# Kernel optimization log

Measured on AMD Instinct MI355X. Metric: run time of the kernel, lower is better.

The kernel has to match this reference:

```python
import jax, jax.numpy as jnp
import numpy as np

B, S, E = 2, 2048, 1024
H, BLK = 16, 32
HD = E // H


def setup_inputs() -> dict:
    key = jax.random.key(0)
    ks = jax.random.split(key, 9)
    s = 1.0 / np.sqrt(E)
    return {
        "x": jax.random.normal(ks[0], (B, S, E), dtype=jnp.float32),
        "Wq": jax.random.normal(ks[1], (E, E), dtype=jnp.float32) * s,
        "bq": jnp.zeros((E,), dtype=jnp.float32),
        "Wk": jax.random.normal(ks[2], (E, E), dtype=jnp.float32) * s,
        "bk": jnp.zeros((E,), dtype=jnp.float32),
        "Wv": jax.random.normal(ks[3], (E, E), dtype=jnp.float32) * s,
        "bv": jnp.zeros((E,), dtype=jnp.float32),
        "Wo": jax.random.normal(ks[4], (E, E), dtype=jnp.float32) * s,
        "bo": jnp.zeros((E,), dtype=jnp.float32),
    }


def reference(x, Wq, bq, Wk, bk, Wv, bv, Wo, bo):
    b, s, e = x.shape
    # projections (torch Linear: x @ W.T + b), split heads -> [b, h, s, hd]
    def proj(W, bias):
        return (x @ W.T + bias).reshape(b, s, H, HD).transpose(0, 2, 1, 3)

    q = proj(Wq, bq)
    k = proj(Wk, bk)
    v = proj(Wv, bv)

    scale = 1.0 / np.sqrt(HD)
    scores = jnp.einsum("bhqd,bhkd->bhqk", q, k) * scale  # [b,h,s,s]

    # block-causal mask: query block i attends to all key blocks j <= i
    idx = jnp.arange(s)
    allowed = (idx[None, :] // BLK) <= (idx[:, None] // BLK)  # [s, s]
    scores = jnp.where(allowed[None, None], scores, jnp.float32(-1e9))

    probs = jax.nn.softmax(scores, axis=-1)
    attn = jnp.einsum("bhqk,bhkd->bhqd", probs, v)  # [b,h,s,hd]
    out = attn.transpose(0, 2, 1, 3).reshape(b, s, e)
    return out @ Wo.T + bo
```

## Files before the change

kernel.cpp:

```cpp
#include <hip/hip_runtime.h>
#include <hip/hip_bf16.h>
#include <stdint.h>

#define BATCH 2
#define S_LEN 2048
#define EMB   1024
#define NHEAD 16
#define HDIM  64

typedef __attribute__((ext_vector_type(8)))  __bf16 bf16x8;
typedef __attribute__((ext_vector_type(4)))  __bf16 bf16x4;
typedef __attribute__((ext_vector_type(4)))  float  f32x4;
typedef __attribute__((ext_vector_type(16))) float  f32x16;

#define ZERO16 ((f32x16){0.f,0.f,0.f,0.f,0.f,0.f,0.f,0.f,0.f,0.f,0.f,0.f,0.f,0.f,0.f,0.f})
#define SM_SCALE_LOG2 0.18033688011112042f

static __device__ __forceinline__ void gload_lds16(const void* g, void* l) {
    __builtin_amdgcn_global_load_lds(
        (__attribute__((address_space(1))) void*)g,
        (__attribute__((address_space(3))) void*)l,
        16, 0, 0);
}

__global__ void f2b_all(const float* __restrict__ x,
                        const float* __restrict__ Wq, const float* __restrict__ Wk,
                        const float* __restrict__ Wv, const float* __restrict__ Wo,
                        __bf16* __restrict__ xb,
                        __bf16* __restrict__ wqb, __bf16* __restrict__ wkb,
                        __bf16* __restrict__ wvb, __bf16* __restrict__ wob) {
    int i = blockIdx.x * blockDim.x + threadIdx.x;
    const float* s;
    __bf16* d;
    int off;
    if (i < (1 << 20)) {
        s = x; d = xb; off = i;
    } else {
        int r   = i - (1 << 20);
        int seg = r >> 18;
        off = r & ((1 << 18) - 1);
        s = seg == 0 ? Wq : seg == 1 ? Wk : seg == 2 ? Wv : Wo;
        d = seg == 0 ? wqb : seg == 1 ? wkb : seg == 2 ? wvb : wob;
    }
    float4 v = reinterpret_cast<const float4*>(s)[off];
    bf16x4 o = { (__bf16)v.x, (__bf16)v.y, (__bf16)v.z, (__bf16)v.w };
    reinterpret_cast<bf16x4*>(d)[off] = o;
}

__global__ __launch_bounds__(256)
void gemm_o64(const __bf16* __restrict__ A, const __bf16* __restrict__ W,
              const float* __restrict__ bias, float* __restrict__ out,
              int M, int N, int K) {
    __shared__ __align__(16) __bf16 As[2][128 * 64];
    __shared__ __align__(16) __bf16 Bs[2][64 * 64];

    const int t    = threadIdx.x;
    const int w    = t >> 6;
    const int lane = t & 63;
    const int m0   = blockIdx.y * 128;
    const int n0   = blockIdx.x * 64;
    const int wr   = w * 32;
    const int fr   = lane & 15;
    const int g16  = lane >> 4;

    f32x4 acc[2][4];
#pragma unroll
    for (int i = 0; i < 2; ++i)
#pragma unroll
        for (int n = 0; n < 4; ++n) acc[i][n] = (f32x4){0.f, 0.f, 0.f, 0.f};

    auto stage = [&](int kt, int buf) {
#pragma unroll
        for (int i = 0; i < 4; ++i) {
            int chunk = i * 256 + t;
            int row   = chunk >> 3;
            int col   = ((chunk & 7) ^ (row & 7)) * 8;
            gload_lds16(A + (size_t)(m0 + row) * K + kt + col,
                        (char*)&As[buf][0] + i * 4096 + w * 1024);
        }
#pragma unroll
        for (int i = 0; i < 2; ++i) {
            int chunk = i * 256 + t;
            int row   = chunk >> 3;
            int col   = ((chunk & 7) ^ (row & 7)) * 8;
            gload_lds16(W + (size_t)(n0 + row) * K + kt + col,
                        (char*)&Bs[buf][0] + i * 4096 + w * 1024);
        }
    };

    stage(0, 0);
    __syncthreads();

    const int NK = K / 64;
    for (int k6 = 0; k6 < NK; ++k6) {
        const int cur = k6 & 1;
        if (k6 + 1 < NK) stage((k6 + 1) * 64, cur ^ 1);

#pragma unroll
        for (int kh = 0; kh < 2; ++kh) {
            bf16x8 af[2], bfv[4];
#pragma unroll
            for (int m = 0; m < 2; ++m) {
                int row = wr + m * 16 + fr;
                int cg  = ((4 * kh + g16) ^ (row & 7)) * 8;
                af[m] = *(const bf16x8*)&As[cur][row * 64 + cg];
            }
#pragma unroll
            for (int n = 0; n < 4; ++n) {
                int row = n * 16 + fr;
                int cg  = ((4 * kh + g16) ^ (row & 7)) * 8;
                bfv[n] = *(const bf16x8*)&Bs[cur][row * 64 + cg];
            }
#pragma unroll
            for (int m = 0; m < 2; ++m)
#pragma unroll
                for (int n = 0; n < 4; ++n)
                    acc[m][n] = __builtin_amdgcn_mfma_f32_16x16x32_bf16(
                        af[m], bfv[n], acc[m][n], 0, 0, 0);
        }
        __syncthreads();
    }

    const int rbase = (lane >> 4) * 4;
#pragma unroll
    for (int m = 0; m < 2; ++m) {
#pragma unroll
        for (int n = 0; n < 4; ++n) {
            int col  = n0 + n * 16 + fr;
            float bv = bias[col];
#pragma unroll
            for (int jj = 0; jj < 4; ++jj) {
                int row = m0 + wr + m * 16 + rbase + jj;
                out[(size_t)row * N + col] = acc[m][n][jj] + bv;
            }
        }
    }
}

__global__ __launch_bounds__(512)
void gemm_qkv(const __bf16* __restrict__ xb,
              const __bf16* __restrict__ Wqb, const __bf16* __restrict__ Wkb,
              const __bf16* __restrict__ Wvb,
              const float* __restrict__ bqp, const float* __restrict__ bkp,
              const float* __restrict__ bvp,
              __bf16* __restrict__ Qo, __bf16* __restrict__ Ko,
              __bf16* __restrict__ VTo, int K) {
    __shared__ __align__(16) __bf16 As[2][128 * 64];
    __shared__ __align__(16) __bf16 Bs[2][128 * 64];

    const int which = blockIdx.x >> 3;
    const int xx    = blockIdx.x & 7;

    const __bf16* Ap;
    const __bf16* Wp;
    int m0, n0;
    if (which == 2) {
        Ap = Wvb; Wp = xb;
        m0 = xx * 128;
        n0 = blockIdx.y * 128;
    } else {
        Ap = xb; Wp = (which == 0) ? Wqb : Wkb;
        m0 = blockIdx.y * 128;
        n0 = xx * 128;
    }
    const float* bias = which == 0 ? bqp : which == 1 ? bkp : bvp;

    const int t    = threadIdx.x;
    const int w    = t >> 6;
    const int lane = t & 63;
    const int wr   = (w >> 2) * 64;
    const int wc   = (w & 3) * 32;
    const int fr   = lane & 15;
    const int g16  = lane >> 4;

    f32x4 acc[4][2];
#pragma unroll
    for (int i = 0; i < 4; ++i)
#pragma unroll
        for (int j = 0; j < 2; ++j) acc[i][j] = (f32x4){0.f, 0.f, 0.f, 0.f};

    auto stage = [&](int kt, int buf) {
#pragma unroll
        for (int i = 0; i < 2; ++i) {
            int chunk = i * 512 + t;
            int row   = chunk >> 3;
            int col   = ((chunk & 7) ^ (row & 7)) * 8;
            gload_lds16(Ap + (size_t)(m0 + row) * K + kt + col,
                        (char*)&As[buf][0] + i * 8192 + w * 1024);
            gload_lds16(Wp + (size_t)(n0 + row) * K + kt + col,
                        (char*)&Bs[buf][0] + i * 8192 + w * 1024);
        }
    };

    stage(0, 0);
    __syncthreads();

    const int NK = K / 64;
    for (int k6 = 0; k6 < NK; ++k6) {
        const int cur = k6 & 1;
        if (k6 + 1 < NK) stage((k6 + 1) * 64, cur ^ 1);

#pragma unroll
        for (int kh = 0; kh < 2; ++kh) {
            bf16x8 af[4], bfv[2];
#pragma unroll
            for (int m = 0; m < 4; ++m) {
                int row = wr + m * 16 + fr;
                int cg  = ((4 * kh + g16) ^ (row & 7)) * 8;
                af[m] = *(const bf16x8*)&As[cur][row * 64 + cg];
            }
#pragma unroll
            for (int n = 0; n < 2; ++n) {
                int row = wc + n * 16 + fr;
                int cg  = ((4 * kh + g16) ^ (row & 7)) * 8;
                bfv[n] = *(const bf16x8*)&Bs[cur][row * 64 + cg];
            }
#pragma unroll
            for (int m = 0; m < 4; ++m)
#pragma unroll
                for (int n = 0; n < 2; ++n)
                    acc[m][n] = __builtin_amdgcn_mfma_f32_16x16x32_bf16(
                        af[m], bfv[n], acc[m][n], 0, 0, 0);
        }
        __syncthreads();
    }

    const int rbase = (lane >> 4) * 4;
    if (which == 2) {
#pragma unroll
        for (int m = 0; m < 4; ++m) {
#pragma unroll
            for (int n = 0; n < 2; ++n) {
                int col = n0 + wc + n * 16 + fr;
                int b   = col >> 11, s = col & (S_LEN - 1);
#pragma unroll
                for (int jj = 0; jj < 4; ++jj) {
                    int row = m0 + wr + m * 16 + rbase + jj;
                    int hh  = row >> 6, d = row & (HDIM - 1);
                    float v = acc[m][n][jj] + bias[row];
                    VTo[(((size_t)(b * NHEAD + hh)) * HDIM + d) * S_LEN + s] = (__bf16)v;
                }
            }
        }
    } else {
        __bf16* outp = (which == 0) ? Qo : Ko;
#pragma unroll
        for (int m = 0; m < 4; ++m) {
#pragma unroll
            for (int n = 0; n < 2; ++n) {
                int col  = n0 + wc + n * 16 + fr;
                float bv = bias[col];
#pragma unroll
                for (int jj = 0; jj < 4; ++jj) {
                    int row = m0 + wr + m * 16 + rbase + jj;
                    float v = acc[m][n][jj] + bv;
                    int b = row >> 11, s = row & (S_LEN - 1);
                    int hh = col >> 6, d = col & (HDIM - 1);
                    outp[(((size_t)(b * NHEAD + hh)) * S_LEN + s) * HDIM + d] = (__bf16)v;
                }
            }
        }
    }
}

__global__ __launch_bounds__(512, 4)
void attn10_kernel(const __bf16* __restrict__ Q, const __bf16* __restrict__ Kv,
                   const __bf16* __restrict__ VT, __bf16* __restrict__ out) {
    __shared__ __align__(16) char smem[51200];
    __bf16* Kt0 = (__bf16*)smem;
    __bf16* Vt  = (__bf16*)(smem + 32768);
    float*  bc  = (float*)(smem + 49152);

    const int t    = threadIdx.x;
    const int w8   = t >> 6;
    const int lane = t & 63;
    const int h    = lane >> 5;
    const int q32  = lane & 31;
    const int j    = w8 & 3;
    const int h2   = w8 >> 2;
    const int bh   = blockIdx.x;
    const int yy   = blockIdx.y;
    const int qt   = (yy < 8) ? (15 - yy) : (yy - 8);
    const int qb   = 4 * qt + j;
    const int C    = qt + 1;

    const __bf16* Qp  = Q  + (size_t)bh * S_LEN * HDIM;
    const __bf16* Kp  = Kv + (size_t)bh * S_LEN * HDIM;
    const __bf16* VTp = VT + (size_t)bh * HDIM * S_LEN;

    const int qrow = qb * 32 + q32;

    bf16x8 qreg[4];
#pragma unroll
    for (int ks = 0; ks < 4; ++ks)
        qreg[ks] = *(const bf16x8*)&Qp[(size_t)qrow * HDIM + 16 * ks + 8 * h];

    f32x16 oacc0 = ZERO16, oacc1 = ZERO16;
    float mrun = -1e30f, lrun = 0.f;

    {
#pragma unroll
        for (int i = 0; i < 2; ++i) {
            int c16 = i * 512 + t;
            int key = c16 >> 3;
            int d0  = ((c16 & 7) ^ (key & 7)) * 8;
            gload_lds16(Kp + (size_t)key * HDIM + d0, (char*)Kt0 + c16 * 16);
        }
        __syncthreads();
    }

    for (int c = 0; c < C; ++c) {
        const int cur = c & 1;
        {
            const int kb = c * 128;
#pragma unroll
            for (int i = 0; i < 2; ++i) {
                int c16 = i * 512 + t;
                int d   = c16 >> 4;
                int o   = c16 & 15;
                gload_lds16(VTp + (size_t)d * S_LEN + kb + ((o ^ (d & 7)) * 8),
                            (char*)Vt + c16 * 16);
            }
        }
        if (c + 1 < C) {
            const int kb = (c + 1) * 128;
#pragma unroll
            for (int i = 0; i < 2; ++i) {
                int c16 = i * 512 + t;
                int key = c16 >> 3;
                int d0  = ((c16 & 7) ^ (key & 7)) * 8;
                gload_lds16(Kp + (size_t)(kb + key) * HDIM + d0,
                            (char*)Kt0 + (cur ^ 1) * 16384 + c16 * 16);
            }
        }

        const int  g0 = 4 * c + 2 * h2;
        const bool w0 = (g0 <= qb);
        const bool w1 = (g0 + 1 <= qb);
        const int  kl0 = 64 * h2;
        const __bf16* Ktc = Kt0 + cur * 8192;

        unsigned L[4], H[4];
        if (w0) {
            f32x16 sac = ZERO16;
            __builtin_amdgcn_s_setprio(1);
#pragma unroll
            for (int ks = 0; ks < 4; ++ks) {
                bf16x8 kf = *(const bf16x8*)&Ktc[(kl0 + q32) * 64 +
                                ((16 * ks + 8 * h) ^ ((q32 & 7) << 3))];
                sac = __builtin_amdgcn_mfma_f32_32x32x16_bf16(kf, qreg[ks], sac, 0, 0, 0);
            }
            __builtin_amdgcn_s_setprio(0);

            float rmax = sac[0];
#pragma unroll
            for (int r = 1; r < 16; ++r) rmax = fmaxf(rmax, sac[r]);
            float pmax = rmax * SM_SCALE_LOG2;
            pmax = fmaxf(pmax, __shfl_xor(pmax, 32));

            if (__any(pmax > mrun + 8.f)) {
                float mnew = fmaxf(mrun, pmax);
                float fac  = exp2f(mrun - mnew);
                mrun = mnew;
                lrun *= fac;
                bc[w8 * 32 + q32] = fac;
                asm volatile("s_waitcnt lgkmcnt(0)" ::: "memory");
                __builtin_amdgcn_sched_barrier(0);
#pragma unroll
                for (int q2 = 0; q2 < 4; ++q2) {
                    f32x4 fv = *(const f32x4*)&bc[w8 * 32 + 8 * q2 + 4 * h];
#pragma unroll
                    for (int jj = 0; jj < 4; ++jj) {
                        oacc0[4 * q2 + jj] *= fv[jj];
                        oacc1[4 * q2 + jj] *= fv[jj];
                    }
                }
            }

            float ps = 0.f;
#pragma unroll
            for (int r = 0; r < 16; ++r) {
                float pv = exp2f(__builtin_fmaf(sac[r], SM_SCALE_LOG2, -mrun));
                ps += pv;
                sac[r] = pv;
            }
            ps += __shfl_xor(ps, 32);
            lrun += ps;

#pragma unroll
            for (int g = 0; g < 4; ++g) {
                asm("v_cvt_pk_bf16_f32 %0, %1, %2"
                    : "=v"(L[g]) : "v"(sac[4 * g]), "v"(sac[4 * g + 1]));
                asm("v_cvt_pk_bf16_f32 %0, %1, %2"
                    : "=v"(H[g]) : "v"(sac[4 * g + 2]), "v"(sac[4 * g + 3]));
            }
        }

        __syncthreads();

        if (w0) {
            __builtin_amdgcn_s_setprio(1);
#pragma unroll
            for (int s2 = 0; s2 < 2; ++s2) {
                unsigned a0 = L[2 * s2], b0 = L[2 * s2 + 1];
                unsigned a1 = H[2 * s2], b1 = H[2 * s2 + 1];
                asm("v_permlane32_swap_b32 %0, %1" : "+v"(a0), "+v"(b0));
                asm("v_permlane32_swap_b32 %0, %1" : "+v"(a1), "+v"(b1));
                unsigned wvw[4] = { a0, a1, b0, b1 };
                bf16x8 pa = *(bf16x8*)wvw;

                const int klb = kl0 + 16 * s2 + 8 * h;
#pragma unroll
                for (int n = 0; n < 2; ++n) {
                    int d = 32 * n + q32;
                    bf16x8 vf = *(const bf16x8*)&Vt[d * 128 +
                                    (klb ^ ((d & 7) << 3))];
                    if (n == 0)
                        oacc0 = __builtin_amdgcn_mfma_f32_32x32x16_bf16(pa, vf, oacc0, 0, 0, 0);
                    else
                        oacc1 = __builtin_amdgcn_mfma_f32_32x32x16_bf16(pa, vf, oacc1, 0, 0, 0);
                }
            }
            __builtin_amdgcn_s_setprio(0);
        }

        if (w1) {
            const int kl1 = kl0 + 32;
            f32x16 sac = ZERO16;
            __builtin_amdgcn_s_setprio(1);
#pragma unroll
            for (int ks = 0; ks < 4; ++ks) {
                bf16x8 kf = *(const bf16x8*)&Ktc[(kl1 + q32) * 64 +
                                ((16 * ks + 8 * h) ^ ((q32 & 7) << 3))];
                sac = __builtin_amdgcn_mfma_f32_32x32x16_bf16(kf, qreg[ks], sac, 0, 0, 0);
            }
            __builtin_amdgcn_s_setprio(0);

            float rmax = sac[0];
#pragma unroll
            for (int r = 1; r < 16; ++r) rmax = fmaxf(rmax, sac[r]);
            float pmax = rmax * SM_SCALE_LOG2;
            pmax = fmaxf(pmax, __shfl_xor(pmax, 32));

            if (__any(pmax > mrun + 8.f)) {
                float mnew = fmaxf(mrun, pmax);
                float fac  = exp2f(mrun - mnew);
                mrun = mnew;
                lrun *= fac;
                bc[w8 * 32 + q32] = fac;
                asm volatile("s_waitcnt lgkmcnt(0)" ::: "memory");
                __builtin_amdgcn_sched_barrier(0);
#pragma unroll
                for (int q2 = 0; q2 < 4; ++q2) {
                    f32x4 fv = *(const f32x4*)&bc[w8 * 32 + 8 * q2 + 4 * h];
#pragma unroll
                    for (int jj = 0; jj < 4; ++jj) {
                        oacc0[4 * q2 + jj] *= fv[jj];
                        oacc1[4 * q2 + jj] *= fv[jj];
                    }
                }
            }

            float ps = 0.f;
#pragma unroll
            for (int r = 0; r < 16; ++r) {
                float pv = exp2f(__builtin_fmaf(sac[r], SM_SCALE_LOG2, -mrun));
                ps += pv;
                sac[r] = pv;
            }
            ps += __shfl_xor(ps, 32);
            lrun += ps;

            unsigned L1[4], H1[4];
#pragma unroll
            for (int g = 0; g < 4; ++g) {
                asm("v_cvt_pk_bf16_f32 %0, %1, %2"
                    : "=v"(L1[g]) : "v"(sac[4 * g]), "v"(sac[4 * g + 1]));
                asm("v_cvt_pk_bf16_f32 %0, %1, %2"
                    : "=v"(H1[g]) : "v"(sac[4 * g + 2]), "v"(sac[4 * g + 3]));
            }

            __builtin_amdgcn_s_setprio(1);
#pragma unroll
            for (int s2 = 0; s2 < 2; ++s2) {
                unsigned a0 = L1[2 * s2], b0 = L1[2 * s2 + 1];
                unsigned a1 = H1[2 * s2], b1 = H1[2 * s2 + 1];
                asm("v_permlane32_swap_b32 %0, %1" : "+v"(a0), "+v"(b0));
                asm("v_permlane32_swap_b32 %0, %1" : "+v"(a1), "+v"(b1));
                unsigned wvw[4] = { a0, a1, b0, b1 };
                bf16x8 pa = *(bf16x8*)wvw;

                const int klb = kl1 + 16 * s2 + 8 * h;
#pragma unroll
                for (int n = 0; n < 2; ++n) {
                    int d = 32 * n + q32;
                    bf16x8 vf = *(const bf16x8*)&Vt[d * 128 +
                                    (klb ^ ((d & 7) << 3))];
                    if (n == 0)
                        oacc0 = __builtin_amdgcn_mfma_f32_32x32x16_bf16(pa, vf, oacc0, 0, 0, 0);
                    else
                        oacc1 = __builtin_amdgcn_mfma_f32_32x32x16_bf16(pa, vf, oacc1, 0, 0, 0);
                }
            }
            __builtin_amdgcn_s_setprio(0);
        }

        __syncthreads();
    }

    float* Oex = (float*)smem;
    float* MLm = (float*)(smem + 49152);
    float* MLl = (float*)(smem + 50176);

    if (h == 0) { MLm[w8 * 32 + q32] = mrun; MLl[w8 * 32 + q32] = lrun; }
    if (h2 == 1) {
        float* ob = Oex + j * 2048;
#pragma unroll
        for (int q2 = 0; q2 < 4; ++q2)
#pragma unroll
            for (int jj = 0; jj < 4; ++jj) {
                int r  = 4 * q2 + jj;
                int rl = 8 * q2 + 4 * h + jj;
                ob[rl * 64 + q32]      = oacc0[r];
                ob[rl * 64 + 32 + q32] = oacc1[r];
            }
    }
    __syncthreads();

    if (h2 == 0) {
        const int b = bh >> 4, hh = bh & (NHEAD - 1);
        __bf16* op = out + (size_t)b * S_LEN * EMB + hh * HDIM;
        const float* ob = Oex + j * 2048;
#pragma unroll
        for (int q2 = 0; q2 < 4; ++q2) {
            f32x4 ma4 = *(const f32x4*)&MLm[j * 32 + 8 * q2 + 4 * h];
            f32x4 mb4 = *(const f32x4*)&MLm[(j + 4) * 32 + 8 * q2 + 4 * h];
            f32x4 la4 = *(const f32x4*)&MLl[j * 32 + 8 * q2 + 4 * h];
            f32x4 lb4 = *(const f32x4*)&MLl[(j + 4) * 32 + 8 * q2 + 4 * h];
#pragma unroll
            for (int jj = 0; jj < 4; ++jj) {
                float ma = ma4[jj], mb = mb4[jj];
                float mst = fmaxf(ma, mb);
                float sa  = exp2f(ma - mst), sb = exp2f(mb - mst);
                float inv = 1.f / (la4[jj] * sa + lb4[jj] * sb);
                int r  = 4 * q2 + jj;
                int rl = 8 * q2 + 4 * h + jj;
                int row = qb * 32 + rl;
                float v0 = (oacc0[r] * sa + ob[rl * 64 + q32] * sb) * inv;
                float v1 = (oacc1[r] * sa + ob[rl * 64 + 32 + q32] * sb) * inv;
                op[(size_t)row * EMB + q32]      = (__bf16)v0;
                op[(size_t)row * EMB + 32 + q32] = (__bf16)v1;
            }
        }
    }
}

extern "C" void kernel_launch(void* const* d_in, const int* in_sizes, int n_in,
                              void* d_out, int out_size, void* d_ws, size_t ws_size,
                              hipStream_t stream) {
    const float* x  = (const float*)d_in[0];
    const float* Wq = (const float*)d_in[1];
    const float* bq = (const float*)d_in[2];
    const float* Wk = (const float*)d_in[3];
    const float* bk = (const float*)d_in[4];
    const float* Wv = (const float*)d_in[5];
    const float* bv = (const float*)d_in[6];
    const float* Wo = (const float*)d_in[7];
    const float* bo = (const float*)d_in[8];
    float* out = (float*)d_out;

    char* ws = (char*)d_ws;
    __bf16* xb  = (__bf16*)(ws + 0);
    __bf16* wqb = (__bf16*)(ws + 8388608);
    __bf16* wkb = (__bf16*)(ws + 10485760);
    __bf16* wvb = (__bf16*)(ws + 12582912);
    __bf16* wob = (__bf16*)(ws + 14680064);
    __bf16* Qb  = (__bf16*)(ws + 16777216);
    __bf16* Kb  = (__bf16*)(ws + 25165824);
    __bf16* VTb = (__bf16*)(ws + 33554432);
    __bf16* Ab  = (__bf16*)(ws + 41943040);

    const int M = BATCH * S_LEN;
    const int N = EMB;
    const int K = EMB;

    f2b_all<<<8192, 256, 0, stream>>>(x, Wq, Wk, Wv, Wo, xb, wqb, wkb, wvb, wob);

    gemm_qkv<<<dim3(24, 32), 512, 0, stream>>>(
        xb, wqb, wkb, wvb, bq, bk, bv, Qb, Kb, VTb, K);

    attn10_kernel<<<dim3(BATCH * NHEAD, 16), 512, 0, stream>>>(Qb, Kb, VTb, Ab);

    gemm_o64<<<dim3(16, M / 128), 256, 0, stream>>>(Ab, wob, bo, out, M, N, K);
}
```

Before: 108.4 us.

## Double-buffer V tiles in attention and drop mid-iteration barrier

The V^T tile is now double-buffered in shared memory alongside K. The next chunk's V is prefetched together with the next K, so the current V load no longer has to finish inside the same iteration. This removes the __syncthreads that separated the QK/softmax phase from the PV phase, and the two duplicated sub-block bodies fold into one unrolled loop with an early break. Shared memory grows from about 50KB to 66KB per block, which may reduce how many blocks fit on each CU.

Measured after the change: 105.0 us. 3.1% less time.

```diff
diff --git a/kernel.cpp b/kernel.cpp
--- a/kernel.cpp
+++ b/kernel.cpp
@@ -264,12 +264,12 @@
 }
 
 __global__ __launch_bounds__(512, 4)
-void attn10_kernel(const __bf16* __restrict__ Q, const __bf16* __restrict__ Kv,
+void attn11_kernel(const __bf16* __restrict__ Q, const __bf16* __restrict__ Kv,
                    const __bf16* __restrict__ VT, __bf16* __restrict__ out) {
-    __shared__ __align__(16) char smem[51200];
+    __shared__ __align__(16) char smem[67584];
     __bf16* Kt0 = (__bf16*)smem;
-    __bf16* Vt  = (__bf16*)(smem + 32768);
-    float*  bc  = (float*)(smem + 49152);
+    __bf16* Vt0 = (__bf16*)(smem + 32768);
+    float*  bc  = (float*)(smem + 65536);
 
     const int t    = threadIdx.x;
     const int w8   = t >> 6;
@@ -306,22 +306,19 @@
             int d0  = ((c16 & 7) ^ (key & 7)) * 8;
             gload_lds16(Kp + (size_t)key * HDIM + d0, (char*)Kt0 + c16 * 16);
         }
+#pragma unroll
+        for (int i = 0; i < 2; ++i) {
+            int c16 = i * 512 + t;
+            int d   = c16 >> 4;
+            int o   = c16 & 15;
+            gload_lds16(VTp + (size_t)d * S_LEN + ((o ^ (d & 7)) * 8),
+                        (char*)Vt0 + c16 * 16);
+        }
         __syncthreads();
     }
 
     for (int c = 0; c < C; ++c) {
         const int cur = c & 1;
-        {
-            const int kb = c * 128;
-#pragma unroll
-            for (int i = 0; i < 2; ++i) {
-                int c16 = i * 512 + t;
-                int d   = c16 >> 4;
-                int o   = c16 & 15;
-                gload_lds16(VTp + (size_t)d * S_LEN + kb + ((o ^ (d & 7)) * 8),
-                            (char*)Vt + c16 * 16);
-            }
-        }
         if (c + 1 < C) {
             const int kb = (c + 1) * 128;
 #pragma unroll
@@ -332,21 +329,30 @@
                 gload_lds16(Kp + (size_t)(kb + key) * HDIM + d0,
                             (char*)Kt0 + (cur ^ 1) * 16384 + c16 * 16);
             }
-        }
-
-        const int  g0 = 4 * c + 2 * h2;
-        const bool w0 = (g0 <= qb);
-        const bool w1 = (g0 + 1 <= qb);
-        const int  kl0 = 64 * h2;
+#pragma unroll
+            for (int i = 0; i < 2; ++i) {
+                int c16 = i * 512 + t;
+                int d   = c16 >> 4;
+                int o   = c16 & 15;
+                gload_lds16(VTp + (size_t)d * S_LEN + kb + ((o ^ (d & 7)) * 8),
+                            (char*)Vt0 + (cur ^ 1) * 16384 + c16 * 16);
+            }
+        }
+
+        const int g0 = 4 * c + 2 * h2;
         const __bf16* Ktc = Kt0 + cur * 8192;
-
-        unsigned L[4], H[4];
-        if (w0) {
+        const __bf16* Vtc = Vt0 + cur * 8192;
+
+#pragma unroll
+        for (int u = 0; u < 2; ++u) {
+            if (g0 + u > qb) break;
+            const int kl = 64 * h2 + 32 * u;
+
             f32x16 sac = ZERO16;
             __builtin_amdgcn_s_setprio(1);
 #pragma unroll
             for (int ks = 0; ks < 4; ++ks) {
-                bf16x8 kf = *(const bf16x8*)&Ktc[(kl0 + q32) * 64 +
+                bf16x8 kf = *(const bf16x8*)&Ktc[(kl + q32) * 64 +
                                 ((16 * ks + 8 * h) ^ ((q32 & 7) << 3))];
                 sac = __builtin_amdgcn_mfma_f32_32x32x16_bf16(kf, qreg[ks], sac, 0, 0, 0);
             }
@@ -387,6 +393,7 @@
             ps += __shfl_xor(ps, 32);
             lrun += ps;
 
+            unsigned L[4], H[4];
 #pragma unroll
             for (int g = 0; g < 4; ++g) {
                 asm("v_cvt_pk_bf16_f32 %0, %1, %2"
@@ -394,11 +401,7 @@
                 asm("v_cvt_pk_bf16_f32 %0, %1, %2"
                     : "=v"(H[g]) : "v"(sac[4 * g + 2]), "v"(sac[4 * g + 3]));
             }
-        }
-
-        __syncthreads();
-
-        if (w0) {
+
             __builtin_amdgcn_s_setprio(1);
 #pragma unroll
             for (int s2 = 0; s2 < 2; ++s2) {
@@ -409,11 +412,11 @@
                 unsigned wvw[4] = { a0, a1, b0, b1 };
                 bf16x8 pa = *(bf16x8*)wvw;
 
-                const int klb = kl0 + 16 * s2 + 8 * h;
+                const int klb = kl + 16 * s2 + 8 * h;
 #pragma unroll
                 for (int n = 0; n < 2; ++n) {
                     int d = 32 * n + q32;
-                    bf16x8 vf = *(const bf16x8*)&Vt[d * 128 +
+                    bf16x8 vf = *(const bf16x8*)&Vtc[d * 128 +
                                     (klb ^ ((d & 7) << 3))];
                     if (n == 0)
                         oacc0 = __builtin_amdgcn_mfma_f32_32x32x16_bf16(pa, vf, oacc0, 0, 0, 0);
@@ -424,93 +427,12 @@
             __builtin_amdgcn_s_setprio(0);
         }
 
-        if (w1) {
-            const int kl1 = kl0 + 32;
-            f32x16 sac = ZERO16;
-            __builtin_amdgcn_s_setprio(1);
-#pragma unroll
-            for (int ks = 0; ks < 4; ++ks) {
-                bf16x8 kf = *(const bf16x8*)&Ktc[(kl1 + q32) * 64 +
-                                ((16 * ks + 8 * h) ^ ((q32 & 7) << 3))];
-                sac = __builtin_amdgcn_mfma_f32_32x32x16_bf16(kf, qreg[ks], sac, 0, 0, 0);
-            }
-            __builtin_amdgcn_s_setprio(0);
-
-            float rmax = sac[0];
-#pragma unroll
-            for (int r = 1; r < 16; ++r) rmax = fmaxf(rmax, sac[r]);
-            float pmax = rmax * SM_SCALE_LOG2;
-            pmax = fmaxf(pmax, __shfl_xor(pmax, 32));
-
-            if (__any(pmax > mrun + 8.f)) {
-                float mnew = fmaxf(mrun, pmax);
-                float fac  = exp2f(mrun - mnew);
-                mrun = mnew;
-                lrun *= fac;
-                bc[w8 * 32 + q32] = fac;
-                asm volatile("s_waitcnt lgkmcnt(0)" ::: "memory");
-                __builtin_amdgcn_sched_barrier(0);
-#pragma unroll
-                for (int q2 = 0; q2 < 4; ++q2) {
-                    f32x4 fv = *(const f32x4*)&bc[w8 * 32 + 8 * q2 + 4 * h];
-#pragma unroll
-                    for (int jj = 0; jj < 4; ++jj) {
-                        oacc0[4 * q2 + jj] *= fv[jj];
-                        oacc1[4 * q2 + jj] *= fv[jj];
-                    }
-                }
-            }
-
-            float ps = 0.f;
-#pragma unroll
-            for (int r = 0; r < 16; ++r) {
-                float pv = exp2f(__builtin_fmaf(sac[r], SM_SCALE_LOG2, -mrun));
-                ps += pv;
-                sac[r] = pv;
-            }
-            ps += __shfl_xor(ps, 32);
-            lrun += ps;
-
-            unsigned L1[4], H1[4];
-#pragma unroll
-            for (int g = 0; g < 4; ++g) {
-                asm("v_cvt_pk_bf16_f32 %0, %1, %2"
-                    : "=v"(L1[g]) : "v"(sac[4 * g]), "v"(sac[4 * g + 1]));
-                asm("v_cvt_pk_bf16_f32 %0, %1, %2"
-                    : "=v"(H1[g]) : "v"(sac[4 * g + 2]), "v"(sac[4 * g + 3]));
-            }
-
-            __builtin_amdgcn_s_setprio(1);
-#pragma unroll
-            for (int s2 = 0; s2 < 2; ++s2) {
-                unsigned a0 = L1[2 * s2], b0 = L1[2 * s2 + 1];
-                unsigned a1 = H1[2 * s2], b1 = H1[2 * s2 + 1];
-                asm("v_permlane32_swap_b32 %0, %1" : "+v"(a0), "+v"(b0));
-                asm("v_permlane32_swap_b32 %0, %1" : "+v"(a1), "+v"(b1));
-                unsigned wvw[4] = { a0, a1, b0, b1 };
-                bf16x8 pa = *(bf16x8*)wvw;
-
-                const int klb = kl1 + 16 * s2 + 8 * h;
-#pragma unroll
-                for (int n = 0; n < 2; ++n) {
-                    int d = 32 * n + q32;
-                    bf16x8 vf = *(const bf16x8*)&Vt[d * 128 +
-                                    (klb ^ ((d & 7) << 3))];
-                    if (n == 0)
-                        oacc0 = __builtin_amdgcn_mfma_f32_32x32x16_bf16(pa, vf, oacc0, 0, 0, 0);
-                    else
-                        oacc1 = __builtin_amdgcn_mfma_f32_32x32x16_bf16(pa, vf, oacc1, 0, 0, 0);
-                }
-            }
-            __builtin_amdgcn_s_setprio(0);
-        }
-
         __syncthreads();
     }
 
     float* Oex = (float*)smem;
-    float* MLm = (float*)(smem + 49152);
-    float* MLl = (float*)(smem + 50176);
+    float* MLm = (float*)(smem + 65536);
+    float* MLl = (float*)(smem + 66560);
 
     if (h == 0) { MLm[w8 * 32 + q32] = mrun; MLl[w8 * 32 + q32] = lrun; }
     if (h2 == 1) {
@@ -589,7 +511,7 @@
     gemm_qkv<<<dim3(24, 32), 512, 0, stream>>>(
         xb, wqb, wkb, wvb, bq, bk, bv, Qb, Kb, VTb, K);
 
-    attn10_kernel<<<dim3(BATCH * NHEAD, 16), 512, 0, stream>>>(Qb, Kb, VTb, Ab);
+    attn11_kernel<<<dim3(BATCH * NHEAD, 16), 512, 0, stream>>>(Qb, Kb, VTb, Ab);
 
     gemm_o64<<<dim3(16, M / 128), 256, 0, stream>>>(Ab, wob, bo, out, M, N, K);
 }
```
